# Kernel optimization log

Hardware: AMD Instinct MI355X
Metric: run time of the kernel (lower is better)

## Reference

```python
import jax, jax.numpy as jnp
import numpy as np
import math

B, N, D, H, A, OBS, NB = 256, 64, 512, 8, 64, 128, 4
HD = D // H
EPS = 1e-5


def layernorm(x, g, b):
    mu = jnp.mean(x, axis=-1, keepdims=True)
    var = jnp.mean((x - mu) ** 2, axis=-1, keepdims=True)
    return (x - mu) * jax.lax.rsqrt(var + EPS) * g + b


def gelu(x):
    return jax.nn.gelu(x, approximate=False)  # torch nn.GELU default = exact erf


def mha_masked(k_in, v_in, q_in, wq, wk, wv, wp, bq, bk, bv, bp):
    # weights stored [in, out]; torch Linear computes x @ W.T, same math with random init
    b, l, d = q_in.shape
    q = (q_in @ wq + bq).reshape(b, l, H, HD).transpose(0, 2, 1, 3)  # [B,H,L,hd]
    k = (k_in @ wk + bk).reshape(b, l, H, HD).transpose(0, 2, 1, 3)
    v = (v_in @ wv + bv).reshape(b, l, H, HD).transpose(0, 2, 1, 3)
    att = jnp.einsum('bhqd,bhkd->bhqk', q, k) * (1.0 / math.sqrt(HD))
    causal = jnp.tril(jnp.ones((l, l), dtype=bool))  # registered tril buffer in original MAT code
    att = jnp.where(causal[None, None], att, -jnp.inf)
    att = jax.nn.softmax(att, axis=-1)
    y = jnp.einsum('bhqk,bhkd->bhqd', att, v)
    y = y.transpose(0, 2, 1, 3).reshape(b, l, d)
    return y @ wp + bp


def setup_inputs() -> dict:
    key = jax.random.key(0)
    ks = iter(jax.random.split(key, 32))
    s = 0.02
    inp = {
        'action': jax.random.normal(next(ks), (B, N, A + 1), jnp.float32),
        'obs_rep': jax.random.normal(next(ks), (B, N, D), jnp.float32),
        'obs': jax.random.normal(next(ks), (B, N, OBS), jnp.float32),
        'w_ae': jax.random.normal(next(ks), (A + 1, D), jnp.float32) * s,
        'ln0_g': jnp.ones((D,), jnp.float32),
        'ln0_b': jnp.zeros((D,), jnp.float32),
        'blk_ln_g': jnp.ones((NB, 3, D), jnp.float32),
        'blk_ln_b': jnp.zeros((NB, 3, D), jnp.float32),
        'blk_wq': jax.random.normal(next(ks), (NB, 2, D, D), jnp.float32) * s,
        'blk_wk': jax.random.normal(next(ks), (NB, 2, D, D), jnp.float32) * s,
        'blk_wv': jax.random.normal(next(ks), (NB, 2, D, D), jnp.float32) * s,
        'blk_wp': jax.random.normal(next(ks), (NB, 2, D, D), jnp.float32) * s,
        'blk_bq': jnp.zeros((NB, 2, D), jnp.float32),
        'blk_bk': jnp.zeros((NB, 2, D), jnp.float32),
        'blk_bv': jnp.zeros((NB, 2, D), jnp.float32),
        'blk_bp': jnp.zeros((NB, 2, D), jnp.float32),
        'blk_w1': jax.random.normal(next(ks), (NB, D, D), jnp.float32) * s,
        'blk_b1': jnp.zeros((NB, D), jnp.float32),
        'blk_w2': jax.random.normal(next(ks), (NB, D, D), jnp.float32) * s,
        'blk_b2': jnp.zeros((NB, D), jnp.float32),
        'wh1': jax.random.normal(next(ks), (D, D), jnp.float32) * s,
        'bh1': jnp.zeros((D,), jnp.float32),
        'lnh_g': jnp.ones((D,), jnp.float32),
        'lnh_b': jnp.zeros((D,), jnp.float32),
        'wh2': jax.random.normal(next(ks), (D, A), jnp.float32) * s,
        'bh2': jnp.zeros((A,), jnp.float32),
    }
    return inp


def reference(action, obs_rep, obs, w_ae, ln0_g, ln0_b, blk_ln_g, blk_ln_b,
              blk_wq, blk_wk, blk_wv, blk_wp, blk_bq, blk_bk, blk_bv, blk_bp,
              blk_w1, blk_b1, blk_w2, blk_b2, wh1, bh1, lnh_g, lnh_b, wh2, bh2):
    # action encoder: Linear(no bias) + GELU, then LayerNorm
    x = layernorm(gelu(action @ w_ae), ln0_g, ln0_b)
    for i in range(NB):
        # sublayer 1: masked self-attn + residual + LN
        a1 = mha_masked(x, x, x, blk_wq[i, 0], blk_wk[i, 0], blk_wv[i, 0], blk_wp[i, 0],
                        blk_bq[i, 0], blk_bk[i, 0], blk_bv[i, 0], blk_bp[i, 0])
        x = layernorm(x + a1, blk_ln_g[i, 0], blk_ln_b[i, 0])
        # sublayer 2: masked cross-attn (key=x, value=x, query=obs_rep) + residual with obs_rep + LN
        a2 = mha_masked(x, x, obs_rep, blk_wq[i, 1], blk_wk[i, 1], blk_wv[i, 1], blk_wp[i, 1],
                        blk_bq[i, 1], blk_bk[i, 1], blk_bv[i, 1], blk_bp[i, 1])
        x = layernorm(obs_rep + a2, blk_ln_g[i, 1], blk_ln_b[i, 1])
        # sublayer 3: GELU MLP (D -> D -> D) + residual + LN
        m = gelu(x @ blk_w1[i] + blk_b1[i]) @ blk_w2[i] + blk_b2[i]
        x = layernorm(x + m, blk_ln_g[i, 2], blk_ln_b[i, 2])
    # head: Linear + GELU + LN + Linear
    h = layernorm(gelu(x @ wh1 + bh1), lnh_g, lnh_b)
    logit = h @ wh2 + bh2
    return logit
```

## Files before the change

### kernel.cpp

```cpp
#include <hip/hip_runtime.h>
#include <hip/hip_bf16.h>
#include <math.h>

namespace {

constexpr int B  = 256;
constexpr int N  = 64;
constexpr int D  = 512;
constexpr int H  = 8;
constexpr int NBLK = 4;
constexpr int M  = B * N;
constexpr float EPS = 1e-5f;
constexpr float SCALE = 0.125f;
constexpr int NEVER = 1 << 20;

typedef __attribute__((ext_vector_type(8))) short short8b;
typedef __attribute__((ext_vector_type(4))) float f32x4;

__device__ __forceinline__ float gelu_exact(float x) {
  return 0.5f * x * (1.0f + erff(x * 0.70710678118654752440f));
}

__device__ __forceinline__ unsigned short f2b_bits(float f) {
  __hip_bfloat16 h = __float2bfloat16(f);
  return *reinterpret_cast<unsigned short*>(&h);
}

#define GLOBAL_AS __attribute__((address_space(1)))
#define LDS_AS    __attribute__((address_space(3)))

__device__ __forceinline__ void gload_lds16(const void* g, void* l) {
  __builtin_amdgcn_global_load_lds((const GLOBAL_AS void*)g, (LDS_AS void*)l, 16, 0, 0);
}

template<bool GELU, int SPLIT>
__global__ __launch_bounds__(512, 2) void gemm_dp_kernel(
    const __hip_bfloat16* __restrict__ A,
    const __hip_bfloat16* __restrict__ Wt,
    const float* __restrict__ bias,
    __hip_bfloat16* __restrict__ out1, int ostr1,
    __hip_bfloat16* __restrict__ vt, int gy) {
  constexpr int K = 512;
  constexpr int NT = 8;
  __shared__ __hip_bfloat16 Als[3][128][64];
  __shared__ __hip_bfloat16 Bls[3][256][64];

  const int nwg = gridDim.x;
  const int hw  = blockIdx.x;
  const int cpx = nwg >> 3;
  const int lg  = (hw & 7) * cpx + (hw >> 3);
  const int bm  = (lg / gy) * 128;
  const int bn  = (lg % gy) * 256;

  const int tid  = threadIdx.x;
  const int wave = tid >> 6;
  const int lane = tid & 63;
  const int wm   = (wave >> 2) * 64;
  const int wn   = (wave & 3) * 64;
  const int fr   = lane & 15;
  const int fg   = lane >> 4;

  const int srow  = tid >> 3;
  const int sslot = (tid & 7) ^ (srow & 7);
  const __hip_bfloat16* gA = A  + (size_t)(bm + srow) * K + sslot * 8;
  const __hip_bfloat16* gB = Wt + (size_t)(bn + srow) * K + sslot * 8;

  auto STAGE = [&](int buf, int kt) {
    const int ko = kt * 64;
    char* la = (char*)&Als[buf][0][0] + wave * 1024;
    char* lb = (char*)&Bls[buf][0][0] + wave * 1024;
    gload_lds16(gA + ko,           la);
    gload_lds16(gA + 64 * K + ko,  la + 8192);
    gload_lds16(gB + ko,           lb);
    gload_lds16(gB + 64 * K + ko,  lb + 8192);
    gload_lds16(gB + 128 * K + ko, lb + 16384);
    gload_lds16(gB + 192 * K + ko, lb + 24576);
  };

  auto lda = [&](int buf, int mi, int ks) -> short8b {
    const int row  = wm + mi * 16 + fr;
    const int byte = row * 128 + (((ks << 2) | fg) ^ (fr & 7)) * 16;
    return *reinterpret_cast<const short8b*>((const char*)&Als[buf][0][0] + byte);
  };
  auto ldb = [&](int buf, int ni, int ks) -> short8b {
    const int row  = wn + ni * 16 + fr;
    const int byte = row * 128 + (((ks << 2) | fg) ^ (fr & 7)) * 16;
    return *reinterpret_cast<const short8b*>((const char*)&Bls[buf][0][0] + byte);
  };

  STAGE(0, 0);
  STAGE(1, 1);
  asm volatile("s_waitcnt vmcnt(6)" ::: "memory");
  __builtin_amdgcn_sched_barrier(0);
  __builtin_amdgcn_s_barrier();
  __builtin_amdgcn_sched_barrier(0);

  f32x4 acc[4][4] = {};
  for (int t = 0; t < NT; ++t) {
    const int cur = t % 3;
    if (t + 2 < NT) STAGE((t + 2) % 3, t + 2);

    short8b a0[4], b0[4], a1[4], b1[4];
#pragma unroll
    for (int mi = 0; mi < 4; ++mi) a0[mi] = lda(cur, mi, 0);
#pragma unroll
    for (int ni = 0; ni < 4; ++ni) b0[ni] = ldb(cur, ni, 0);
#pragma unroll
    for (int mi = 0; mi < 4; ++mi) a1[mi] = lda(cur, mi, 1);
#pragma unroll
    for (int ni = 0; ni < 4; ++ni) b1[ni] = ldb(cur, ni, 1);

    __builtin_amdgcn_s_setprio(1);
#pragma unroll
    for (int mi = 0; mi < 4; ++mi)
#pragma unroll
      for (int ni = 0; ni < 4; ++ni)
        acc[mi][ni] = __builtin_amdgcn_mfma_f32_16x16x32_bf16(a0[mi], b0[ni], acc[mi][ni], 0, 0, 0);
#pragma unroll
    for (int mi = 0; mi < 4; ++mi)
#pragma unroll
      for (int ni = 0; ni < 4; ++ni)
        acc[mi][ni] = __builtin_amdgcn_mfma_f32_16x16x32_bf16(a1[mi], b1[ni], acc[mi][ni], 0, 0, 0);
    __builtin_amdgcn_s_setprio(0);

    if (t + 2 < NT) {
      asm volatile("s_waitcnt vmcnt(6)" ::: "memory");
    } else {
      asm volatile("s_waitcnt vmcnt(0)" ::: "memory");
    }
    __builtin_amdgcn_sched_barrier(0);
    __builtin_amdgcn_s_barrier();
    __builtin_amdgcn_sched_barrier(0);
  }

#pragma unroll
  for (int ni = 0; ni < 4; ++ni) {
    const int col = bn + wn + ni * 16 + fr;
    const float bv = bias ? bias[col] : 0.f;
#pragma unroll
    for (int mi = 0; mi < 4; ++mi) {
      const int row0 = bm + wm + mi * 16 + fg * 4;
      if (col >= SPLIT) {
        const int vcol = col - SPLIT;
        ushort4 o;
        o.x = f2b_bits(acc[mi][ni][0] + bv);
        o.y = f2b_bits(acc[mi][ni][1] + bv);
        o.z = f2b_bits(acc[mi][ni][2] + bv);
        o.w = f2b_bits(acc[mi][ni][3] + bv);
        const int b8 = row0 >> 6, nl = row0 & 63;
        const int hh = vcol >> 6, dl = vcol & 63;
        *reinterpret_cast<ushort4*>(vt +
            ((size_t)(b8 * 8 + hh) * 4096 + dl * 64 + nl)) = o;
      } else {
#pragma unroll
        for (int q = 0; q < 4; ++q) {
          float v = acc[mi][ni][q] + bv;
          if (GELU) v = gelu_exact(v);
          out1[(size_t)(row0 + q) * ostr1 + col] = __float2bfloat16(v);
        }
      }
    }
  }
}

template<bool GELU_PRE, bool RES>
__global__ __launch_bounds__(512) void gemm_ln64_kernel(
    const __hip_bfloat16* __restrict__ A,
    const __hip_bfloat16* __restrict__ Wt,
    const float* __restrict__ bias,
    const __hip_bfloat16* __restrict__ resb,
    const float* __restrict__ g, const float* __restrict__ bb,
    __hip_bfloat16* __restrict__ outB) {
  __shared__ __hip_bfloat16 Als[2][64][64];
  __shared__ __hip_bfloat16 Bls[2][512][64];
  __shared__ float red[64][8];
  __shared__ float mrow[64];
  __shared__ float rrow[64];

  const int bm   = blockIdx.x * 64;
  const int tid  = threadIdx.x;
  const int wave = tid >> 6;
  const int lane = tid & 63;
  const int fr   = lane & 15;
  const int fg   = lane >> 4;

  const int srow  = tid >> 3;
  const int sslot = (tid & 7) ^ (srow & 7);

  auto stage = [&](int buf, int kt) {
    const int ko = kt * 64;
    gload_lds16(A + (size_t)(bm + srow) * 512 + ko + sslot * 8,
                (char*)&Als[buf][0][0] + wave * 1024);
#pragma unroll
    for (int j = 0; j < 8; ++j) {
      const int row = j * 64 + srow;
      const int sl  = (tid & 7) ^ (row & 7);
      gload_lds16(Wt + (size_t)row * 512 + ko + sl * 8,
                  (char*)&Bls[buf][0][0] + j * 8192 + wave * 1024);
    }
  };

  auto lda = [&](int buf, int mi, int ks) -> short8b {
    const int row  = mi * 16 + fr;
    const int byte = row * 128 + (((ks << 2) | fg) ^ (row & 7)) * 16;
    return *reinterpret_cast<const short8b*>((const char*)&Als[buf][0][0] + byte);
  };
  auto ldb = [&](int buf, int ni, int ks) -> short8b {
    const int row  = wave * 64 + ni * 16 + fr;
    const int byte = row * 128 + (((ks << 2) | fg) ^ (row & 7)) * 16;
    return *reinterpret_cast<const short8b*>((const char*)&Bls[buf][0][0] + byte);
  };

  f32x4 acc[4][4] = {};
  stage(0, 0);
  int buf = 0;
  for (int kt = 0; kt < 8; ++kt) {
    __syncthreads();
    if (kt + 1 < 8) stage(buf ^ 1, kt + 1);
    short8b a0[4], b0[4], a1[4], b1[4];
#pragma unroll
    for (int mi = 0; mi < 4; ++mi) a0[mi] = lda(buf, mi, 0);
#pragma unroll
    for (int ni = 0; ni < 4; ++ni) b0[ni] = ldb(buf, ni, 0);
#pragma unroll
    for (int mi = 0; mi < 4; ++mi) a1[mi] = lda(buf, mi, 1);
#pragma unroll
    for (int ni = 0; ni < 4; ++ni) b1[ni] = ldb(buf, ni, 1);
    __builtin_amdgcn_s_setprio(1);
#pragma unroll
    for (int mi = 0; mi < 4; ++mi)
#pragma unroll
      for (int ni = 0; ni < 4; ++ni)
        acc[mi][ni] = __builtin_amdgcn_mfma_f32_16x16x32_bf16(a0[mi], b0[ni], acc[mi][ni], 0, 0, 0);
#pragma unroll
    for (int mi = 0; mi < 4; ++mi)
#pragma unroll
      for (int ni = 0; ni < 4; ++ni)
        acc[mi][ni] = __builtin_amdgcn_mfma_f32_16x16x32_bf16(a1[mi], b1[ni], acc[mi][ni], 0, 0, 0);
    __builtin_amdgcn_s_setprio(0);
    buf ^= 1;
  }

  float v[4][4][4];
  float bvc[4];
#pragma unroll
  for (int ni = 0; ni < 4; ++ni)
    bvc[ni] = bias ? bias[wave * 64 + ni * 16 + fr] : 0.f;
#pragma unroll
  for (int mi = 0; mi < 4; ++mi)
#pragma unroll
    for (int q = 0; q < 4; ++q) {
      const int row = bm + mi * 16 + fg * 4 + q;
#pragma unroll
      for (int ni = 0; ni < 4; ++ni) {
        float t = acc[mi][ni][q] + bvc[ni];
        if (GELU_PRE) t = gelu_exact(t);
        if (RES)
          t += __bfloat162float(resb[(size_t)row * D + wave * 64 + ni * 16 + fr]);
        v[mi][ni][q] = t;
      }
    }

  float ps[16];
#pragma unroll
  for (int mi = 0; mi < 4; ++mi)
#pragma unroll
    for (int q = 0; q < 4; ++q)
      ps[mi * 4 + q] = v[mi][0][q] + v[mi][1][q] + v[mi][2][q] + v[mi][3][q];
#pragma unroll
  for (int mask = 1; mask < 16; mask <<= 1)
#pragma unroll
    for (int t = 0; t < 16; ++t) ps[t] += __shfl_xor(ps[t], mask);
  if (fr == 0) {
#pragma unroll
    for (int mi = 0; mi < 4; ++mi)
#pragma unroll
      for (int q = 0; q < 4; ++q)
        red[mi * 16 + fg * 4 + q][wave] = ps[mi * 4 + q];
  }
  __syncthreads();
  if (tid < 64) {
    float s = 0.f;
#pragma unroll
    for (int w = 0; w < 8; ++w) s += red[tid][w];
    mrow[tid] = s * (1.f / 512.f);
  }
  __syncthreads();
  float mu[16];
#pragma unroll
  for (int mi = 0; mi < 4; ++mi)
#pragma unroll
    for (int q = 0; q < 4; ++q) mu[mi * 4 + q] = mrow[mi * 16 + fg * 4 + q];

  float ps2[16];
#pragma unroll
  for (int mi = 0; mi < 4; ++mi)
#pragma unroll
    for (int q = 0; q < 4; ++q) {
      const float m = mu[mi * 4 + q];
      float s = 0.f;
#pragma unroll
      for (int ni = 0; ni < 4; ++ni) {
        const float d = v[mi][ni][q] - m;
        s += d * d;
      }
      ps2[mi * 4 + q] = s;
    }
#pragma unroll
  for (int mask = 1; mask < 16; mask <<= 1)
#pragma unroll
    for (int t = 0; t < 16; ++t) ps2[t] += __shfl_xor(ps2[t], mask);
  if (fr == 0) {
#pragma unroll
    for (int mi = 0; mi < 4; ++mi)
#pragma unroll
      for (int q = 0; q < 4; ++q)
        red[mi * 16 + fg * 4 + q][wave] = ps2[mi * 4 + q];
  }
  __syncthreads();
  if (tid < 64) {
    float s = 0.f;
#pragma unroll
    for (int w = 0; w < 8; ++w) s += red[tid][w];
    rrow[tid] = rsqrtf(s * (1.f / 512.f) + EPS);
  }
  __syncthreads();

#pragma unroll
  for (int ni = 0; ni < 4; ++ni) {
    const int col = wave * 64 + ni * 16 + fr;
    const float gc = g[col], bc = bb[col];
#pragma unroll
    for (int mi = 0; mi < 4; ++mi)
#pragma unroll
      for (int q = 0; q < 4; ++q) {
        const int lrow = mi * 16 + fg * 4 + q;
        const float o = (v[mi][ni][q] - mu[mi * 4 + q]) * rrow[lrow] * gc + bc;
        outB[(size_t)(bm + lrow) * D + col] = __float2bfloat16(o);
      }
  }
}

template<int KSTEPS>
__global__ __launch_bounds__(256) void gemm_head_kernel(
    const __hip_bfloat16* __restrict__ A,
    const __hip_bfloat16* __restrict__ Wt,
    const float* __restrict__ bias,
    float* __restrict__ out1, int ostr1, int nvalid) {
  constexpr int K = KSTEPS * 32;
  __shared__ __hip_bfloat16 Als[2][128][32];
  __shared__ __hip_bfloat16 Bls[2][128][32];

  const int bm   = blockIdx.x * 128;
  const int bn   = blockIdx.y * 128;
  const int tid  = threadIdx.x;
  const int wave = tid >> 6;
  const int lane = tid & 63;
  const int wm   = (wave >> 1) * 64;
  const int wn   = (wave & 1) * 64;
  const int fr   = lane & 15;
  const int fg   = lane >> 4;

  const int srow = (lane >> 2);
  const int scol = (lane & 3) * 8;
  const __hip_bfloat16* gA0 = A  + (size_t)(bm + wave * 32 + srow) * K + scol;
  const __hip_bfloat16* gA1 = gA0 + 16 * K;
  const __hip_bfloat16* gB0 = Wt + (size_t)(bn + wave * 32 + srow) * K + scol;
  const __hip_bfloat16* gB1 = gB0 + 16 * K;

  f32x4 acc[4][4] = {};

  auto stage = [&](int buf, int ks) {
    const int ko = ks * 32;
    gload_lds16(gA0 + ko, &Als[buf][wave * 32][0]);
    gload_lds16(gA1 + ko, &Als[buf][wave * 32 + 16][0]);
    gload_lds16(gB0 + ko, &Bls[buf][wave * 32][0]);
    gload_lds16(gB1 + ko, &Bls[buf][wave * 32 + 16][0]);
  };

  stage(0, 0);
  int buf = 0;
  for (int ks = 0; ks < KSTEPS; ++ks) {
    __syncthreads();
    if (ks + 1 < KSTEPS) stage(buf ^ 1, ks + 1);
    short8b a[4], b[4];
#pragma unroll
    for (int mi = 0; mi < 4; ++mi)
      a[mi] = *reinterpret_cast<const short8b*>(&Als[buf][wm + mi * 16 + fr][fg * 8]);
#pragma unroll
    for (int ni = 0; ni < 4; ++ni)
      b[ni] = *reinterpret_cast<const short8b*>(&Bls[buf][wn + ni * 16 + fr][fg * 8]);
#pragma unroll
    for (int mi = 0; mi < 4; ++mi)
#pragma unroll
      for (int ni = 0; ni < 4; ++ni)
        acc[mi][ni] = __builtin_amdgcn_mfma_f32_16x16x32_bf16(a[mi], b[ni], acc[mi][ni], 0, 0, 0);
    buf ^= 1;
  }

#pragma unroll
  for (int ni = 0; ni < 4; ++ni) {
    const int col = bn + wn + ni * 16 + fr;
    if (col >= nvalid) continue;
    const float bv = bias ? bias[col] : 0.f;
#pragma unroll
    for (int mi = 0; mi < 4; ++mi) {
      const int row0 = bm + wm + mi * 16 + fg * 4;
#pragma unroll
      for (int q = 0; q < 4; ++q)
        out1[(size_t)(row0 + q) * ostr1 + col] = acc[mi][ni][q] + bv;
    }
  }
}

__global__ __launch_bounds__(512) void gemm_ln_enc_kernel(
    const __hip_bfloat16* __restrict__ A,
    const __hip_bfloat16* __restrict__ Wt,
    const float* __restrict__ g, const float* __restrict__ bb,
    __hip_bfloat16* __restrict__ outB) {
  constexpr int K = 96;
  __shared__ __hip_bfloat16 Als[2][64][32];
  __shared__ __hip_bfloat16 Bls[2][512][32];
  __shared__ float red[64][8];
  __shared__ float mrow[64];
  __shared__ float rrow[64];

  const int bm   = blockIdx.x * 64;
  const int tid  = threadIdx.x;
  const int wave = tid >> 6;
  const int lane = tid & 63;
  const int fr   = lane & 15;
  const int fg   = lane >> 4;
  const int srow = lane >> 2;
  const int scol = (lane & 3) * 8;

  auto stage = [&](int buf, int ks) {
    const int ko = ks * 32;
    if (wave < 4)
      gload_lds16(A + (size_t)(bm + wave * 16 + srow) * K + ko + scol,
                  &Als[buf][wave * 16][0]);
#pragma unroll
    for (int c = 0; c < 4; ++c)
      gload_lds16(Wt + (size_t)(wave * 64 + c * 16 + srow) * K + ko + scol,
                  &Bls[buf][wave * 64 + c * 16][0]);
  };

  f32x4 acc[4][4] = {};
  stage(0, 0);
  int buf = 0;
  for (int ks = 0; ks < 3; ++ks) {
    __syncthreads();
    if (ks + 1 < 3) stage(buf ^ 1, ks + 1);
    short8b a[4], b[4];
#pragma unroll
    for (int mi = 0; mi < 4; ++mi)
      a[mi] = *reinterpret_cast<const short8b*>(&Als[buf][mi * 16 + fr][fg * 8]);
#pragma unroll
    for (int ni = 0; ni < 4; ++ni)
      b[ni] = *reinterpret_cast<const short8b*>(&Bls[buf][wave * 64 + ni * 16 + fr][fg * 8]);
#pragma unroll
    for (int mi = 0; mi < 4; ++mi)
#pragma unroll
      for (int ni = 0; ni < 4; ++ni)
        acc[mi][ni] = __builtin_amdgcn_mfma_f32_16x16x32_bf16(a[mi], b[ni], acc[mi][ni], 0, 0, 0);
    buf ^= 1;
  }

  float v[4][4][4];
#pragma unroll
  for (int mi = 0; mi < 4; ++mi)
#pragma unroll
    for (int q = 0; q < 4; ++q)
#pragma unroll
      for (int ni = 0; ni < 4; ++ni)
        v[mi][ni][q] = gelu_exact(acc[mi][ni][q]);

  float ps[16];
#pragma unroll
  for (int mi = 0; mi < 4; ++mi)
#pragma unroll
    for (int q = 0; q < 4; ++q)
      ps[mi * 4 + q] = v[mi][0][q] + v[mi][1][q] + v[mi][2][q] + v[mi][3][q];
#pragma unroll
  for (int mask = 1; mask < 16; mask <<= 1)
#pragma unroll
    for (int t = 0; t < 16; ++t) ps[t] += __shfl_xor(ps[t], mask);
  if (fr == 0)
#pragma unroll
    for (int mi = 0; mi < 4; ++mi)
#pragma unroll
      for (int q = 0; q < 4; ++q)
        red[mi * 16 + fg * 4 + q][wave] = ps[mi * 4 + q];
  __syncthreads();
  if (tid < 64) {
    float s = 0.f;
#pragma unroll
    for (int w = 0; w < 8; ++w) s += red[tid][w];
    mrow[tid] = s * (1.f / 512.f);
  }
  __syncthreads();
  float mu[16];
#pragma unroll
  for (int mi = 0; mi < 4; ++mi)
#pragma unroll
    for (int q = 0; q < 4; ++q) mu[mi * 4 + q] = mrow[mi * 16 + fg * 4 + q];
  float ps2[16];
#pragma unroll
  for (int mi = 0; mi < 4; ++mi)
#pragma unroll
    for (int q = 0; q < 4; ++q) {
      const float m = mu[mi * 4 + q];
      float s = 0.f;
#pragma unroll
      for (int ni = 0; ni < 4; ++ni) { const float d = v[mi][ni][q] - m; s += d * d; }
      ps2[mi * 4 + q] = s;
    }
#pragma unroll
  for (int mask = 1; mask < 16; mask <<= 1)
#pragma unroll
    for (int t = 0; t < 16; ++t) ps2[t] += __shfl_xor(ps2[t], mask);
  if (fr == 0)
#pragma unroll
    for (int mi = 0; mi < 4; ++mi)
#pragma unroll
      for (int q = 0; q < 4; ++q)
        red[mi * 16 + fg * 4 + q][wave] = ps2[mi * 4 + q];
  __syncthreads();
  if (tid < 64) {
    float s = 0.f;
#pragma unroll
    for (int w = 0; w < 8; ++w) s += red[tid][w];
    rrow[tid] = rsqrtf(s * (1.f / 512.f) + EPS);
  }
  __syncthreads();

#pragma unroll
  for (int ni = 0; ni < 4; ++ni) {
    const int col = wave * 64 + ni * 16 + fr;
    const float gc = g[col], bc = bb[col];
#pragma unroll
    for (int mi = 0; mi < 4; ++mi)
#pragma unroll
      for (int q = 0; q < 4; ++q) {
        const int lrow = mi * 16 + fg * 4 + q;
        const float o = (v[mi][ni][q] - mu[mi * 4 + q]) * rrow[lrow] * gc + bc;
        outB[(size_t)(bm + lrow) * D + col] = __float2bfloat16(o);
      }
  }
}

__global__ __launch_bounds__(256) void attn_mfma_kernel(
    const __hip_bfloat16* __restrict__ qg, int qstr,
    const __hip_bfloat16* __restrict__ kg, int kstr,
    const __hip_bfloat16* __restrict__ vt,
    __hip_bfloat16* __restrict__ yg) {
  __shared__ __align__(16) char smem[33280];
  unsigned short* Qs  = (unsigned short*)smem;
  unsigned short* Ks  = (unsigned short*)(smem + 8192);
  float*          Ss  = (float*)smem;
  unsigned short* Vts = (unsigned short*)(smem + 16896);
  unsigned short* Ps  = (unsigned short*)(smem + 25088);

  const int tid  = threadIdx.x;
  const int bh   = blockIdx.x;
  const int bidx = bh >> 3, h = bh & 7;
  const size_t rbase = (size_t)bidx * 64;
  const int col0 = h * 64;

  const __hip_bfloat16* vtg = vt + (size_t)bh * 4096;
#pragma unroll
  for (int p = 0; p < 2; ++p) {
    const int idx = tid + p * 256;
    const int row = idx >> 3, c8 = (idx & 7) * 8;
    const int lb  = (row * 128 + c8 * 2) ^ ((row & 7) << 4);
    const uint4 vq = *reinterpret_cast<const uint4*>(qg + (rbase + row) * qstr + col0 + c8);
    const uint4 vk = *reinterpret_cast<const uint4*>(kg + (rbase + row) * kstr + col0 + c8);
    const uint4 vv = *reinterpret_cast<const uint4*>(vtg + idx * 8);
    *reinterpret_cast<uint4*>((char*)Qs  + lb) = vq;
    *reinterpret_cast<uint4*>((char*)Ks  + lb) = vk;
    *reinterpret_cast<uint4*>((char*)Vts + lb) = vv;
  }
  __syncthreads();

  const int wave = tid >> 6, lane = tid & 63;
  const int fr = lane & 15, fg = lane >> 4;
  const int wr = (wave >> 1) * 32, wc = (wave & 1) * 32;

  auto ldfrag = [&](const unsigned short* base, int row, int ks) -> short8b {
    const int byte = (row * 128 + ks * 64 + fg * 16) ^ ((row & 7) << 4);
    return *reinterpret_cast<const short8b*>((const char*)base + byte);
  };

  f32x4 acc[2][2] = {};
#pragma unroll
  for (int ks = 0; ks < 2; ++ks) {
    short8b a[2], b[2];
    a[0] = ldfrag(Qs, wr + fr, ks);
    a[1] = ldfrag(Qs, wr + 16 + fr, ks);
    b[0] = ldfrag(Ks, wc + fr, ks);
    b[1] = ldfrag(Ks, wc + 16 + fr, ks);
#pragma unroll
    for (int mi = 0; mi < 2; ++mi)
#pragma unroll
      for (int ni = 0; ni < 2; ++ni)
        acc[mi][ni] = __builtin_amdgcn_mfma_f32_16x16x32_bf16(a[mi], b[ni], acc[mi][ni], 0, 0, 0);
  }
  __syncthreads();

#pragma unroll
  for (int mi = 0; mi < 2; ++mi)
#pragma unroll
    for (int ni = 0; ni < 2; ++ni) {
      const int m2 = wc + ni * 16 + fr;
#pragma unroll
      for (int r = 0; r < 4; ++r) {
        const int n = wr + mi * 16 + fg * 4 + r;
        Ss[n * 66 + m2] = (m2 <= n) ? acc[mi][ni][r] * SCALE : -1e30f;
      }
    }
  __syncthreads();

  for (int n = wave * 16; n < wave * 16 + 16; ++n) {
    const float vv = Ss[n * 66 + lane];
    float mx = vv;
#pragma unroll
    for (int off = 1; off < 64; off <<= 1) mx = fmaxf(mx, __shfl_xor(mx, off));
    const float p = (lane <= n) ? __expf(vv - mx) : 0.f;
    float sum = p;
#pragma unroll
    for (int off = 1; off < 64; off <<= 1) sum += __shfl_xor(sum, off);
    const int byte = (n * 128 + lane * 2) ^ ((n & 7) << 4);
    *(unsigned short*)((char*)Ps + byte) = f2b_bits(p / sum);
  }
  __syncthreads();

  f32x4 acc2[2][2] = {};
#pragma unroll
  for (int ks = 0; ks < 2; ++ks) {
    short8b a[2], b[2];
    a[0] = ldfrag(Ps, wr + fr, ks);
    a[1] = ldfrag(Ps, wr + 16 + fr, ks);
    b[0] = ldfrag(Vts, wc + fr, ks);
    b[1] = ldfrag(Vts, wc + 16 + fr, ks);
#pragma unroll
    for (int mi = 0; mi < 2; ++mi)
#pragma unroll
      for (int ni = 0; ni < 2; ++ni)
        acc2[mi][ni] = __builtin_amdgcn_mfma_f32_16x16x32_bf16(a[mi], b[ni], acc2[mi][ni], 0, 0, 0);
  }
#pragma unroll
  for (int mi = 0; mi < 2; ++mi)
#pragma unroll
    for (int r = 0; r < 4; ++r) {
      const int n = wr + mi * 16 + fg * 4 + r;
      yg[(rbase + n) * 512 + col0 + wc + fr]      = __float2bfloat16(acc2[mi][0][r]);
      yg[(rbase + n) * 512 + col0 + wc + 16 + fr] = __float2bfloat16(acc2[mi][1][r]);
    }
}

__global__ __launch_bounds__(256) void wconv_all_kernel(
    const float* __restrict__ bwq, const float* __restrict__ bwk,
    const float* __restrict__ bwv, const float* __restrict__ bwp,
    const float* __restrict__ bw1, const float* __restrict__ bw2,
    const float* __restrict__ wh1,
    __hip_bfloat16* __restrict__ wSelf, __hip_bfloat16* __restrict__ wCq,
    __hip_bfloat16* __restrict__ wCkv, __hip_bfloat16* __restrict__ wTp,
    __hip_bfloat16* __restrict__ wTw1, __hip_bfloat16* __restrict__ wTw2,
    __hip_bfloat16* __restrict__ wTh1) {
  const size_t MAT = (size_t)D * D;
  const size_t SS = (size_t)1536 * 512, KV = (size_t)1024 * 512;
  const int z = blockIdx.z;
  const float* src;
  __hip_bfloat16* dst;
  if (z < 8)       { int i = z >> 1; src = bwq + (size_t)z * MAT;
                     dst = (z & 1) ? wCq + (size_t)i * MAT : wSelf + (size_t)i * SS; }
  else if (z < 16) { int zz = z - 8, i = zz >> 1; src = bwk + (size_t)zz * MAT;
                     dst = (zz & 1) ? wCkv + (size_t)i * KV
                                    : wSelf + (size_t)i * SS + 512 * 512; }
  else if (z < 24) { int zz = z - 16, i = zz >> 1; src = bwv + (size_t)zz * MAT;
                     dst = (zz & 1) ? wCkv + (size_t)i * KV + 512 * 512
                                    : wSelf + (size_t)i * SS + 1024 * 512; }
  else if (z < 32) { int zz = z - 24; src = bwp + (size_t)zz * MAT; dst = wTp + (size_t)zz * MAT; }
  else if (z < 36) { int zz = z - 32; src = bw1 + (size_t)zz * MAT; dst = wTw1 + (size_t)zz * MAT; }
  else if (z < 40) { int zz = z - 36; src = bw2 + (size_t)zz * MAT; dst = wTw2 + (size_t)zz * MAT; }
  else             { src = wh1; dst = wTh1; }

  __shared__ float tile[32][33];
  const int r0 = blockIdx.y * 32, c0 = blockIdx.x * 32;
  const int tr = threadIdx.x >> 5;
  const int tc = threadIdx.x & 31;
#pragma unroll
  for (int i = 0; i < 4; ++i)
    tile[tr + 8 * i][tc] = src[(size_t)(r0 + tr + 8 * i) * D + c0 + tc];
  __syncthreads();
#pragma unroll
  for (int i = 0; i < 4; ++i)
    dst[(size_t)(c0 + tr + 8 * i) * D + r0 + tc] = __float2bfloat16(tile[tc][tr + 8 * i]);
}

__global__ __launch_bounds__(256) void misc_prep_kernel(
    const float* __restrict__ w_ae, const float* __restrict__ wh2,
    const float* __restrict__ bbq, const float* __restrict__ bbk,
    const float* __restrict__ bbv, const float* __restrict__ action,
    const float* __restrict__ obs_rep,
    __hip_bfloat16* __restrict__ waeT, __hip_bfloat16* __restrict__ wh2p,
    float* __restrict__ selfb, float* __restrict__ ckvb,
    float* __restrict__ bqc, __hip_bfloat16* __restrict__ actb,
    __hip_bfloat16* __restrict__ orb) {
  constexpr int R0 = 512 * 96, R1 = 128 * 512, R2 = NBLK * 1536,
                R3 = NBLK * 1024, R4 = NBLK * 512, R5 = M * 96;
  constexpr int R6 = M * D / 4;
  constexpr int total = R0 + R1 + R2 + R3 + R4 + R5 + R6;
  for (int i = blockIdx.x * 256 + threadIdx.x; i < total; i += gridDim.x * 256) {
    int j = i;
    if (j < R0) {
      const int n = j / 96, k = j - n * 96;
      waeT[j] = (k < 65) ? __float2bfloat16(w_ae[(size_t)k * 512 + n]) : __float2bfloat16(0.f);
    } else if ((j -= R0) < R1) {
      const int n = j >> 9, k = j & 511;
      wh2p[j] = (n < 64) ? __float2bfloat16(wh2[(size_t)k * 64 + n]) : __float2bfloat16(0.f);
    } else if ((j -= R1) < R2) {
      const int blk = j / 1536, c = j - blk * 1536;
      const int seg = c >> 9, cc = c & 511;
      const float* s = (seg == 0) ? bbq : (seg == 1) ? bbk : bbv;
      selfb[j] = s[(size_t)(blk * 2) * 512 + cc];
    } else if ((j -= R2) < R3) {
      const int blk = j >> 10, c = j & 1023;
      ckvb[j] = (c < 512) ? bbk[(size_t)(blk * 2 + 1) * 512 + c]
                          : bbv[(size_t)(blk * 2 + 1) * 512 + (c - 512)];
    } else if ((j -= R3) < R4) {
      const int blk = j >> 9, c = j & 511;
      bqc[j] = bbq[(size_t)(blk * 2 + 1) * 512 + c];
    } else if ((j -= R4) < R5) {
      const int row = j / 96, k = j - row * 96;
      actb[j] = (k < 65) ? __float2bfloat16(action[(size_t)row * 65 + k]) : __float2bfloat16(0.f);
    } else {
      j -= R5;
      const float4 v = reinterpret_cast<const float4*>(obs_rep)[j];
      ushort4 o;
      o.x = f2b_bits(v.x); o.y = f2b_bits(v.y);
      o.z = f2b_bits(v.z); o.w = f2b_bits(v.w);
      reinterpret_cast<ushort4*>(orb)[j] = o;
    }
  }
}

}

extern "C" void kernel_launch(void* const* d_in, const int* in_sizes, int n_in,
                              void* d_out, int out_size, void* d_ws, size_t ws_size,
                              hipStream_t stream) {
  const float* action  = (const float*)d_in[0];
  const float* obs_rep = (const float*)d_in[1];
  const float* w_ae    = (const float*)d_in[3];
  const float* ln0_g   = (const float*)d_in[4];
  const float* ln0_b   = (const float*)d_in[5];
  const float* bln_g   = (const float*)d_in[6];
  const float* bln_b   = (const float*)d_in[7];
  const float* bwq     = (const float*)d_in[8];
  const float* bwk     = (const float*)d_in[9];
  const float* bwv     = (const float*)d_in[10];
  const float* bwp     = (const float*)d_in[11];
  const float* bbq     = (const float*)d_in[12];
  const float* bbk     = (const float*)d_in[13];
  const float* bbv     = (const float*)d_in[14];
  const float* bbp     = (const float*)d_in[15];
  const float* bw1     = (const float*)d_in[16];
  const float* bb1     = (const float*)d_in[17];
  const float* bw2     = (const float*)d_in[18];
  const float* bb2     = (const float*)d_in[19];
  const float* wh1     = (const float*)d_in[20];
  const float* bh1     = (const float*)d_in[21];
  const float* lnh_g   = (const float*)d_in[22];
  const float* lnh_b   = (const float*)d_in[23];
  const float* wh2     = (const float*)d_in[24];
  const float* bh2     = (const float*)d_in[25];

  char* ws = (char*)d_ws;
  const size_t MAT = (size_t)D * D;
  const size_t szB = (size_t)M * D * 2;

  __hip_bfloat16* xb  = (__hip_bfloat16*)ws; ws += szB;
  __hip_bfloat16* hb  = (__hip_bfloat16*)ws; ws += szB;
  __hip_bfloat16* vtb = (__hip_bfloat16*)ws; ws += szB;
  __hip_bfloat16* orb = (__hip_bfloat16*)ws; ws += szB;
  __hip_bfloat16* qkb = (__hip_bfloat16*)ws; ws += 2 * szB;
  __hip_bfloat16* qcb = (__hip_bfloat16*)ws; ws += 4 * szB;
  __hip_bfloat16* kb  = (__hip_bfloat16*)ws; ws += szB;
  __hip_bfloat16* actb = (__hip_bfloat16*)ws; ws += (size_t)M * 96 * 2;
  __hip_bfloat16* wSelf = (__hip_bfloat16*)ws; ws += (size_t)NBLK * 1536 * 512 * 2;
  __hip_bfloat16* wCq   = (__hip_bfloat16*)ws; ws += (size_t)NBLK * 512 * 512 * 2;
  __hip_bfloat16* wCkv  = (__hip_bfloat16*)ws; ws += (size_t)NBLK * 1024 * 512 * 2;
  __hip_bfloat16* wTp   = (__hip_bfloat16*)ws; ws += 8 * MAT * 2;
  __hip_bfloat16* wTw1  = (__hip_bfloat16*)ws; ws += 4 * MAT * 2;
  __hip_bfloat16* wTw2  = (__hip_bfloat16*)ws; ws += 4 * MAT * 2;
  __hip_bfloat16* wTh1  = (__hip_bfloat16*)ws; ws += MAT * 2;
  __hip_bfloat16* wh2p  = (__hip_bfloat16*)ws; ws += 128 * 512 * 2;
  __hip_bfloat16* waeT  = (__hip_bfloat16*)ws; ws += 512 * 96 * 2;
  float* selfb         = (float*)ws;         ws += (size_t)NBLK * 1536 * 4;
  float* ckvb          = (float*)ws;         ws += (size_t)NBLK * 1024 * 4;
  float* bqc           = (float*)ws;         ws += (size_t)NBLK * 512 * 4;

  wconv_all_kernel<<<dim3(16, 16, 41), 256, 0, stream>>>(
      bwq, bwk, bwv, bwp, bw1, bw2, wh1,
      wSelf, wCq, wCkv, wTp, wTw1, wTw2, wTh1);
  misc_prep_kernel<<<2048, 256, 0, stream>>>(
      w_ae, wh2, bbq, bbk, bbv, action, obs_rep,
      waeT, wh2p, selfb, ckvb, bqc, actb, orb);

  const size_t SS = (size_t)1536 * 512;
  const size_t KV = (size_t)1024 * 512;
  const int lnGrid = M / 64;

  gemm_ln_enc_kernel<<<lnGrid, 512, 0, stream>>>(actb, waeT, ln0_g, ln0_b, xb);

  gemm_dp_kernel<false, NEVER><<<M / 128 * 8, 512, 0, stream>>>(
      orb, wCq, bqc, qcb, 2048, nullptr, 8);

  for (int i = 0; i < NBLK; ++i) {
    const float* g0 = bln_g + (size_t)(i * 3 + 0) * D;
    const float* b0 = bln_b + (size_t)(i * 3 + 0) * D;
    const float* g1 = bln_g + (size_t)(i * 3 + 1) * D;
    const float* b1 = bln_b + (size_t)(i * 3 + 1) * D;
    const float* g2 = bln_g + (size_t)(i * 3 + 2) * D;
    const float* b2 = bln_b + (size_t)(i * 3 + 2) * D;

    gemm_dp_kernel<false, 1024><<<M / 128 * 6, 512, 0, stream>>>(
        xb, wSelf + (size_t)i * SS, selfb + (size_t)i * 1536, qkb, 1024, vtb, 6);
    attn_mfma_kernel<<<B * H, 256, 0, stream>>>(qkb, 1024, qkb + 512, 1024, vtb, hb);
    gemm_ln64_kernel<false, true><<<lnGrid, 512, 0, stream>>>(
        hb, wTp + (size_t)(i * 2) * MAT, bbp + (size_t)(i * 2) * D, xb, g0, b0, xb);

    gemm_dp_kernel<false, 512><<<M / 128 * 4, 512, 0, stream>>>(
        xb, wCkv + (size_t)i * KV, ckvb + (size_t)i * 1024, kb, 512, vtb, 4);
    attn_mfma_kernel<<<B * H, 256, 0, stream>>>(
        qcb + (size_t)i * 512, 2048, kb, 512, vtb, hb);
    gemm_ln64_kernel<false, true><<<lnGrid, 512, 0, stream>>>(
        hb, wTp + (size_t)(i * 2 + 1) * MAT, bbp + (size_t)(i * 2 + 1) * D,
        orb, g1, b1, xb);

    gemm_dp_kernel<true, NEVER><<<M / 128 * 2, 512, 0, stream>>>(
        xb, wTw1 + (size_t)i * MAT, bb1 + (size_t)i * D, hb, 512, nullptr, 2);
    gemm_ln64_kernel<false, true><<<lnGrid, 512, 0, stream>>>(
        hb, wTw2 + (size_t)i * MAT, bb2 + (size_t)i * D, xb, g2, b2, xb);
  }

  gemm_ln64_kernel<true, false><<<lnGrid, 512, 0, stream>>>(
      xb, wTh1, bh1, nullptr, lnh_g, lnh_b, hb);
  gemm_head_kernel<16><<<dim3(M / 128, 1), 256, 0, stream>>>(
      hb, wh2p, bh2, (float*)d_out, 64, 64);
}
```

Before: 998.5 us.

## Add 256x256-tile double-buffered GEMM with staged half-tile prefetch for projections

```diff
diff --git a/kernel.cpp b/kernel.cpp
--- a/kernel.cpp
+++ b/kernel.cpp
@@ -31,6 +31,167 @@
 
 __device__ __forceinline__ void gload_lds16(const void* g, void* l) {
   __builtin_amdgcn_global_load_lds((const GLOBAL_AS void*)g, (LDS_AS void*)l, 16, 0, 0);
+}
+
+__device__ __forceinline__ void barrier_pinned() {
+  __builtin_amdgcn_sched_barrier(0);
+  __builtin_amdgcn_s_barrier();
+  __builtin_amdgcn_sched_barrier(0);
+}
+
+template<bool GELU, int SPLIT>
+__global__ __launch_bounds__(512, 2) void gemm_dp2_kernel(
+    const __hip_bfloat16* __restrict__ A,
+    const __hip_bfloat16* __restrict__ Wt,
+    const float* __restrict__ bias,
+    __hip_bfloat16* __restrict__ out1, int ostr1,
+    __hip_bfloat16* __restrict__ vt, int gy) {
+  constexpr int K = 512;
+  constexpr int NT = 8;
+  __shared__ __hip_bfloat16 Als[2][256][64];
+  __shared__ __hip_bfloat16 Bls[2][256][64];
+
+  const int nwg = gridDim.x;
+  const int hw  = blockIdx.x;
+  const int cpx = nwg >> 3;
+  const int lg  = (hw & 7) * cpx + (hw >> 3);
+  const int bm  = (lg / gy) * 256;
+  const int bn  = (lg % gy) * 256;
+
+  const int tid  = threadIdx.x;
+  const int wave = tid >> 6;
+  const int lane = tid & 63;
+  const int wm   = (wave >> 2) * 128;
+  const int wn   = (wave & 3) * 64;
+  const int fr   = lane & 15;
+  const int fg   = lane >> 4;
+
+  const int srow  = tid >> 3;
+  const int sslot = (tid & 7) ^ (srow & 7);
+  const __hip_bfloat16* gA = A  + (size_t)(bm + srow) * K + sslot * 8;
+  const __hip_bfloat16* gB = Wt + (size_t)(bn + srow) * K + sslot * 8;
+
+  auto STAGE_A = [&](int buf, int kt, int h) {
+    const int ko = kt * 64;
+    char* l = (char*)&Als[buf][h * 128][0] + wave * 1024;
+    gload_lds16(gA + (size_t)(h * 128) * K + ko,      l);
+    gload_lds16(gA + (size_t)(h * 128 + 64) * K + ko, l + 8192);
+  };
+  auto STAGE_B = [&](int buf, int kt, int h) {
+    const int ko = kt * 64;
+    char* l = (char*)&Bls[buf][h * 128][0] + wave * 1024;
+    gload_lds16(gB + (size_t)(h * 128) * K + ko,      l);
+    gload_lds16(gB + (size_t)(h * 128 + 64) * K + ko, l + 8192);
+  };
+
+  auto lda = [&](int buf, int mi, int kh) -> short8b {
+    const int row  = wm + mi * 16 + fr;
+    const int byte = row * 128 + (((kh << 2) | fg) ^ (fr & 7)) * 16;
+    return *reinterpret_cast<const short8b*>((const char*)&Als[buf][0][0] + byte);
+  };
+  auto ldb = [&](int buf, int ni, int kh) -> short8b {
+    const int row  = wn + ni * 16 + fr;
+    const int byte = row * 128 + (((kh << 2) | fg) ^ (fr & 7)) * 16;
+    return *reinterpret_cast<const short8b*>((const char*)&Bls[buf][0][0] + byte);
+  };
+
+  STAGE_A(0, 0, 0); STAGE_A(0, 0, 1);
+  STAGE_B(0, 0, 0); STAGE_B(0, 0, 1);
+
+  f32x4 acc[8][4] = {};
+  short8b a[4][2], b[4][2];
+
+  for (int t = 0; t < NT; ++t) {
+    const int cur = t & 1, nxt = cur ^ 1;
+    const bool pre = (t + 1 < NT);
+
+    if (pre) STAGE_A(nxt, t + 1, 0);
+    if (pre) { asm volatile("s_waitcnt vmcnt(2)" ::: "memory"); }
+    else     { asm volatile("s_waitcnt vmcnt(0)" ::: "memory"); }
+    barrier_pinned();
+#pragma unroll
+    for (int mi = 0; mi < 4; ++mi) { a[mi][0] = lda(cur, mi, 0); a[mi][1] = lda(cur, mi, 1); }
+#pragma unroll
+    for (int ni = 0; ni < 2; ++ni) { b[ni][0] = ldb(cur, ni, 0); b[ni][1] = ldb(cur, ni, 1); }
+    __builtin_amdgcn_s_setprio(1);
+#pragma unroll
+    for (int kh = 0; kh < 2; ++kh)
+#pragma unroll
+      for (int mi = 0; mi < 4; ++mi)
+#pragma unroll
+        for (int ni = 0; ni < 2; ++ni)
+          acc[mi][ni] = __builtin_amdgcn_mfma_f32_16x16x32_bf16(a[mi][kh], b[ni][kh], acc[mi][ni], 0, 0, 0);
+    __builtin_amdgcn_s_setprio(0);
+
+    if (pre) STAGE_A(nxt, t + 1, 1);
+    barrier_pinned();
+#pragma unroll
+    for (int ni = 2; ni < 4; ++ni) { b[ni][0] = ldb(cur, ni, 0); b[ni][1] = ldb(cur, ni, 1); }
+    __builtin_amdgcn_s_setprio(1);
+#pragma unroll
+    for (int kh = 0; kh < 2; ++kh)
+#pragma unroll
+      for (int mi = 0; mi < 4; ++mi)
+#pragma unroll
+        for (int ni = 2; ni < 4; ++ni)
+          acc[mi][ni] = __builtin_amdgcn_mfma_f32_16x16x32_bf16(a[mi][kh], b[ni][kh], acc[mi][ni], 0, 0, 0);
+    __builtin_amdgcn_s_setprio(0);
+
+    if (pre) STAGE_B(nxt, t + 1, 0);
+    barrier_pinned();
+#pragma unroll
+    for (int mi = 0; mi < 4; ++mi) { a[mi][0] = lda(cur, mi + 4, 0); a[mi][1] = lda(cur, mi + 4, 1); }
+    __builtin_amdgcn_s_setprio(1);
+#pragma unroll
+    for (int kh = 0; kh < 2; ++kh)
+#pragma unroll
+      for (int mi = 0; mi < 4; ++mi)
+#pragma unroll
+        for (int ni = 0; ni < 2; ++ni)
+          acc[mi + 4][ni] = __builtin_amdgcn_mfma_f32_16x16x32_bf16(a[mi][kh], b[ni][kh], acc[mi + 4][ni], 0, 0, 0);
+    __builtin_amdgcn_s_setprio(0);
+
+    if (pre) STAGE_B(nxt, t + 1, 1);
+    barrier_pinned();
+    __builtin_amdgcn_s_setprio(1);
+#pragma unroll
+    for (int kh = 0; kh < 2; ++kh)
+#pragma unroll
+      for (int mi = 0; mi < 4; ++mi)
+#pragma unroll
+        for (int ni = 2; ni < 4; ++ni)
+          acc[mi + 4][ni] = __builtin_amdgcn_mfma_f32_16x16x32_bf16(a[mi][kh], b[ni][kh], acc[mi + 4][ni], 0, 0, 0);
+    __builtin_amdgcn_s_setprio(0);
+  }
+
+#pragma unroll
+  for (int ni = 0; ni < 4; ++ni) {
+    const int col = bn + wn + ni * 16 + fr;
+    const float bv = bias ? bias[col] : 0.f;
+#pragma unroll
+    for (int mi = 0; mi < 8; ++mi) {
+      const int row0 = bm + wm + mi * 16 + fg * 4;
+      if (col >= SPLIT) {
+        const int vcol = col - SPLIT;
+        ushort4 o;
+        o.x = f2b_bits(acc[mi][ni][0] + bv);
+        o.y = f2b_bits(acc[mi][ni][1] + bv);
+        o.z = f2b_bits(acc[mi][ni][2] + bv);
+        o.w = f2b_bits(acc[mi][ni][3] + bv);
+        const int b8 = row0 >> 6, nl = row0 & 63;
+        const int hh = vcol >> 6, dl = vcol & 63;
+        *reinterpret_cast<ushort4*>(vt +
+            ((size_t)(b8 * 8 + hh) * 4096 + dl * 64 + nl)) = o;
+      } else {
+#pragma unroll
+        for (int q = 0; q < 4; ++q) {
+          float v = acc[mi][ni][q] + bv;
+          if (GELU) v = gelu_exact(v);
+          out1[(size_t)(row0 + q) * ostr1 + col] = __float2bfloat16(v);
+        }
+      }
+    }
+  }
 }
 
 template<bool GELU, int SPLIT>
@@ -91,9 +252,7 @@
   STAGE(0, 0);
   STAGE(1, 1);
   asm volatile("s_waitcnt vmcnt(6)" ::: "memory");
-  __builtin_amdgcn_sched_barrier(0);
-  __builtin_amdgcn_s_barrier();
-  __builtin_amdgcn_sched_barrier(0);
+  barrier_pinned();
 
   f32x4 acc[4][4] = {};
   for (int t = 0; t < NT; ++t) {
@@ -128,9 +287,7 @@
     } else {
       asm volatile("s_waitcnt vmcnt(0)" ::: "memory");
     }
-    __builtin_amdgcn_sched_barrier(0);
-    __builtin_amdgcn_s_barrier();
-    __builtin_amdgcn_sched_barrier(0);
+    barrier_pinned();
   }
 
 #pragma unroll
@@ -814,7 +971,7 @@
 
   gemm_ln_enc_kernel<<<lnGrid, 512, 0, stream>>>(actb, waeT, ln0_g, ln0_b, xb);
 
-  gemm_dp_kernel<false, NEVER><<<M / 128 * 8, 512, 0, stream>>>(
+  gemm_dp2_kernel<false, NEVER><<<M / 256 * 8, 512, 0, stream>>>(
       orb, wCq, bqc, qcb, 2048, nullptr, 8);
 
   for (int i = 0; i < NBLK; ++i) {
@@ -825,13 +982,13 @@
     const float* g2 = bln_g + (size_t)(i * 3 + 2) * D;
     const float* b2 = bln_b + (size_t)(i * 3 + 2) * D;
 
-    gemm_dp_kernel<false, 1024><<<M / 128 * 6, 512, 0, stream>>>(
+    gemm_dp2_kernel<false, 1024><<<M / 256 * 6, 512, 0, stream>>>(
         xb, wSelf + (size_t)i * SS, selfb + (size_t)i * 1536, qkb, 1024, vtb, 6);
     attn_mfma_kernel<<<B * H, 256, 0, stream>>>(qkb, 1024, qkb + 512, 1024, vtb, hb);
     gemm_ln64_kernel<false, true><<<lnGrid, 512, 0, stream>>>(
         hb, wTp + (size_t)(i * 2) * MAT, bbp + (size_t)(i * 2) * D, xb, g0, b0, xb);
 
-    gemm_dp_kernel<false, 512><<<M / 128 * 4, 512, 0, stream>>>(
+    gemm_dp2_kernel<false, 512><<<M / 256 * 4, 512, 0, stream>>>(
         xb, wCkv + (size_t)i * KV, ckvb + (size_t)i * 1024, kb, 512, vtb, 4);
     attn_mfma_kernel<<<B * H, 256, 0, stream>>>(
         qcb + (size_t)i * 512, 2048, kb, 512, vtb, hb);
```

New measurement: 1.025 ms. +2.7%, slower.

## Add 256x256-tile GEMM with 4-deep k32 staging for QKV projections

Applied to the files above, without the earlier changes.

```diff
diff --git a/kernel.cpp b/kernel.cpp
--- a/kernel.cpp
+++ b/kernel.cpp
@@ -31,6 +31,119 @@
 
 __device__ __forceinline__ void gload_lds16(const void* g, void* l) {
   __builtin_amdgcn_global_load_lds((const GLOBAL_AS void*)g, (LDS_AS void*)l, 16, 0, 0);
+}
+
+__device__ __forceinline__ void barrier_pinned() {
+  __builtin_amdgcn_sched_barrier(0);
+  __builtin_amdgcn_s_barrier();
+  __builtin_amdgcn_sched_barrier(0);
+}
+
+template<bool GELU, int SPLIT>
+__global__ __launch_bounds__(512) void gemm_dp2b_kernel(
+    const __hip_bfloat16* __restrict__ A,
+    const __hip_bfloat16* __restrict__ Wt,
+    const float* __restrict__ bias,
+    __hip_bfloat16* __restrict__ out1, int ostr1,
+    __hip_bfloat16* __restrict__ vt, int gy) {
+  constexpr int K = 512;
+  constexpr int NS = 16;
+  __shared__ __align__(16) char lds[4][32768];
+
+  const int nwg = gridDim.x;
+  const int hw  = blockIdx.x;
+  const int cpx = nwg >> 3;
+  const int lg  = (hw & 7) * cpx + (hw >> 3);
+  const int bm  = (lg / gy) * 256;
+  const int bn  = (lg % gy) * 256;
+
+  const int tid  = threadIdx.x;
+  const int wave = tid >> 6;
+  const int lane = tid & 63;
+  const int wm   = (wave >> 2) * 128;
+  const int wn   = (wave & 3) * 64;
+  const int fr   = lane & 15;
+  const int fg   = lane >> 4;
+
+  const int strow0 = wave * 16 + (lane >> 2);
+
+  auto STAGE = [&](int s) {
+    const int buf = s & 3;
+    const int ko  = (s >> 1) * 64 + (s & 1) * 32;
+#pragma unroll
+    for (int r = 0; r < 2; ++r) {
+      const int row = r * 128 + strow0;
+      const int sl  = (lane & 3) ^ (row & 3);
+      gload_lds16(A  + (size_t)(bm + row) * K + ko + sl * 8,
+                  &lds[buf][r * 8192 + wave * 1024]);
+      gload_lds16(Wt + (size_t)(bn + row) * K + ko + sl * 8,
+                  &lds[buf][16384 + r * 8192 + wave * 1024]);
+    }
+  };
+
+  auto ldA = [&](int s, int row) -> short8b {
+    const int byte = row * 64 + ((fg ^ (row & 3)) << 4);
+    return *reinterpret_cast<const short8b*>(&lds[s & 3][byte]);
+  };
+  auto ldB = [&](int s, int row) -> short8b {
+    const int byte = 16384 + row * 64 + ((fg ^ (row & 3)) << 4);
+    return *reinterpret_cast<const short8b*>(&lds[s & 3][byte]);
+  };
+
+  STAGE(0);
+  STAGE(1);
+
+  f32x4 acc[8][4] = {};
+  for (int s = 0; s < NS; ++s) {
+    if (s + 2 < NS) STAGE(s + 2);
+    if (s + 2 < NS)      { asm volatile("s_waitcnt vmcnt(8)" ::: "memory"); }
+    else if (s + 1 < NS) { asm volatile("s_waitcnt vmcnt(4)" ::: "memory"); }
+    else                 { asm volatile("s_waitcnt vmcnt(0)" ::: "memory"); }
+    barrier_pinned();
+
+    short8b af[8], bf_[4];
+#pragma unroll
+    for (int mi = 0; mi < 8; ++mi) af[mi] = ldA(s, wm + mi * 16 + fr);
+#pragma unroll
+    for (int ni = 0; ni < 4; ++ni) bf_[ni] = ldB(s, wn + ni * 16 + fr);
+
+    __builtin_amdgcn_s_setprio(1);
+#pragma unroll
+    for (int mi = 0; mi < 8; ++mi)
+#pragma unroll
+      for (int ni = 0; ni < 4; ++ni)
+        acc[mi][ni] = __builtin_amdgcn_mfma_f32_16x16x32_bf16(af[mi], bf_[ni], acc[mi][ni], 0, 0, 0);
+    __builtin_amdgcn_s_setprio(0);
+  }
+
+#pragma unroll
+  for (int ni = 0; ni < 4; ++ni) {
+    const int col = bn + wn + ni * 16 + fr;
+    const float bv = bias ? bias[col] : 0.f;
+#pragma unroll
+    for (int mi = 0; mi < 8; ++mi) {
+      const int row0 = bm + wm + mi * 16 + fg * 4;
+      if (col >= SPLIT) {
+        const int vcol = col - SPLIT;
+        ushort4 o;
+        o.x = f2b_bits(acc[mi][ni][0] + bv);
+        o.y = f2b_bits(acc[mi][ni][1] + bv);
+        o.z = f2b_bits(acc[mi][ni][2] + bv);
+        o.w = f2b_bits(acc[mi][ni][3] + bv);
+        const int b8 = row0 >> 6, nl = row0 & 63;
+        const int hh = vcol >> 6, dl = vcol & 63;
+        *reinterpret_cast<ushort4*>(vt +
+            ((size_t)(b8 * 8 + hh) * 4096 + dl * 64 + nl)) = o;
+      } else {
+#pragma unroll
+        for (int q = 0; q < 4; ++q) {
+          float v = acc[mi][ni][q] + bv;
+          if (GELU) v = gelu_exact(v);
+          out1[(size_t)(row0 + q) * ostr1 + col] = __float2bfloat16(v);
+        }
+      }
+    }
+  }
 }
 
 template<bool GELU, int SPLIT>
@@ -91,9 +204,7 @@
   STAGE(0, 0);
   STAGE(1, 1);
   asm volatile("s_waitcnt vmcnt(6)" ::: "memory");
-  __builtin_amdgcn_sched_barrier(0);
-  __builtin_amdgcn_s_barrier();
-  __builtin_amdgcn_sched_barrier(0);
+  barrier_pinned();
 
   f32x4 acc[4][4] = {};
   for (int t = 0; t < NT; ++t) {
@@ -128,9 +239,7 @@
     } else {
       asm volatile("s_waitcnt vmcnt(0)" ::: "memory");
     }
-    __builtin_amdgcn_sched_barrier(0);
-    __builtin_amdgcn_s_barrier();
-    __builtin_amdgcn_sched_barrier(0);
+    barrier_pinned();
   }
 
 #pragma unroll
@@ -814,7 +923,7 @@
 
   gemm_ln_enc_kernel<<<lnGrid, 512, 0, stream>>>(actb, waeT, ln0_g, ln0_b, xb);
 
-  gemm_dp_kernel<false, NEVER><<<M / 128 * 8, 512, 0, stream>>>(
+  gemm_dp2b_kernel<false, NEVER><<<M / 256 * 8, 512, 0, stream>>>(
       orb, wCq, bqc, qcb, 2048, nullptr, 8);
 
   for (int i = 0; i < NBLK; ++i) {
@@ -825,13 +934,13 @@
     const float* g2 = bln_g + (size_t)(i * 3 + 2) * D;
     const float* b2 = bln_b + (size_t)(i * 3 + 2) * D;
 
-    gemm_dp_kernel<false, 1024><<<M / 128 * 6, 512, 0, stream>>>(
+    gemm_dp2b_kernel<false, 1024><<<M / 256 * 6, 512, 0, stream>>>(
         xb, wSelf + (size_t)i * SS, selfb + (size_t)i * 1536, qkb, 1024, vtb, 6);
     attn_mfma_kernel<<<B * H, 256, 0, stream>>>(qkb, 1024, qkb + 512, 1024, vtb, hb);
     gemm_ln64_kernel<false, true><<<lnGrid, 512, 0, stream>>>(
         hb, wTp + (size_t)(i * 2) * MAT, bbp + (size_t)(i * 2) * D, xb, g0, b0, xb);
 
-    gemm_dp_kernel<false, 512><<<M / 128 * 4, 512, 0, stream>>>(
+    gemm_dp2b_kernel<false, 512><<<M / 256 * 4, 512, 0, stream>>>(
         xb, wCkv + (size_t)i * KV, ckvb + (size_t)i * 1024, kb, 512, vtb, 4);
     attn_mfma_kernel<<<B * H, 256, 0, stream>>>(
         qcb + (size_t)i * 512, 2048, kb, 512, vtb, hb);
```

Result: slower. 1.045 ms (+4.7%).
